# Kernel optimization log

Measured on AMD Instinct MI355X. Metric: run time of the kernel, lower is better.

The kernel has to match this reference:

```python
import jax, jax.numpy as jnp
import numpy as np

EPS = 1e-5
K = 9
DILATION = 1

def bn(x, g, b, m, v):
    # x: (B,C,N,1), inference-mode BatchNorm2d with running stats
    sh = (1, -1, 1, 1)
    return (x - m.reshape(sh)) * (g.reshape(sh) / jnp.sqrt(v.reshape(sh) + EPS)) + b.reshape(sh)

def conv1x1(x, w, b):
    # w: (Cout, Cin), x: (B,Cin,N,1)
    return jnp.einsum('oc,bcnj->bonj', w, x) + b.reshape(1, -1, 1, 1)

def knn_idx(feat, k):
    # feat: (B,C,N) -> (B,N,k) indices of k nearest nodes (incl. self)
    xt = jnp.transpose(feat, (0, 2, 1))  # (B,N,C)
    x2 = jnp.sum(xt * xt, axis=-1)       # (B,N)
    dist = x2[:, :, None] - 2.0 * jnp.einsum('bnc,bmc->bnm', xt, xt) + x2[:, None, :]
    _, idx = jax.lax.top_k(-dist, k)
    return idx

def setup_inputs():
    key = jax.random.key(0)
    ks = jax.random.split(key, 24)
    B, C, H, W = 16, 256, 32, 32
    HID = 512
    def g(i, shape, s=1.0):
        return jax.random.normal(ks[i], shape, dtype=jnp.float32) * s
    def pos(i, shape):
        return jax.random.uniform(ks[i], shape, dtype=jnp.float32, minval=0.5, maxval=1.5)
    return {
        'x': g(0, (B, C, H, W)),
        'fc1_w': g(1, (C, C), 0.05), 'fc1_b': g(2, (C,), 0.05),
        'bn1_g': pos(3, (C,)), 'bn1_b': g(4, (C,), 0.1), 'bn1_m': g(5, (C,), 0.1), 'bn1_v': pos(6, (C,)),
        'gc_w': g(7, (HID, 2 * C), 0.05), 'gc_b': g(8, (HID,), 0.05),
        'gbn_g': pos(9, (HID,)), 'gbn_b': g(10, (HID,), 0.1), 'gbn_m': g(11, (HID,), 0.1), 'gbn_v': pos(12, (HID,)),
        'bn2_g': pos(13, (HID,)), 'bn2_b': g(14, (HID,), 0.1), 'bn2_m': g(15, (HID,), 0.1), 'bn2_v': pos(16, (HID,)),
        'fc2_w': g(17, (C, HID), 0.05), 'fc2_b': g(18, (C,), 0.05),
        'bn3_g': pos(19, (C,)), 'bn3_b': g(20, (C,), 0.1), 'bn3_m': g(21, (C,), 0.1), 'bn3_v': pos(22, (C,)),
    }

def reference(x, fc1_w, fc1_b, bn1_g, bn1_b, bn1_m, bn1_v,
              gc_w, gc_b, gbn_g, gbn_b, gbn_m, gbn_v,
              bn2_g, bn2_b, bn2_m, bn2_v,
              fc2_w, fc2_b, bn3_g, bn3_b, bn3_m, bn3_v):
    B, C, H, W = x.shape
    N = H * W
    x = x.reshape(B, C, N, 1)
    shortcut = x
    # fc1: 1x1 conv + BN
    h = bn(conv1x1(x, fc1_w, fc1_b), bn1_g, bn1_b, bn1_m, bn1_v)
    # DyGraphConv2d: dynamic dilated kNN graph over N nodes
    feat = h[..., 0]  # (B,C,N)
    idx = knn_idx(feat, K * DILATION)[:, :, ::DILATION]  # (B,N,K)
    # MRConv2d: max over neighbors of (x_j - x_i)
    x_j = jax.vmap(lambda f, i: f[:, i])(feat, idx)        # (B,C,N,K) gather
    diff_max = jnp.max(x_j - feat[:, :, :, None], axis=-1)  # (B,C,N)
    # interleave [x, max_diff] along channel dim -> (B, 2C, N, 1)
    m = jnp.stack([feat, diff_max], axis=2).reshape(B, 2 * C, N, 1)
    g = conv1x1(m, gc_w, gc_b)
    g = bn(g, gbn_g, gbn_b, gbn_m, gbn_v)  # BasicConv BN, act='None'
    # graph_conv Sequential: BN + GELU (erf, torch default)
    g = jax.nn.gelu(bn(g, bn2_g, bn2_b, bn2_m, bn2_v), approximate=False)
    # fc2 + residual (drop_path=0 -> identity)
    out = bn(conv1x1(g, fc2_w, fc2_b), bn3_g, bn3_b, bn3_m, bn3_v)
    return out + shortcut
```

## Files before the change

kernel.cpp:

```cpp
#include <hip/hip_runtime.h>
#include <hip/hip_bf16.h>
#include <stdint.h>

typedef unsigned long long u64;
typedef __hip_bfloat16 bf16;
typedef short s8v __attribute__((ext_vector_type(8)));
typedef short s4v __attribute__((ext_vector_type(4)));
typedef float f4v __attribute__((ext_vector_type(4)));

#define B_   16
#define C_   256
#define N_   1024
#define HID_ 512

__device__ __forceinline__ unsigned short f2b(float f) {
    unsigned u = __float_as_uint(f);
    unsigned r = (u + 0x7FFFu + ((u >> 16) & 1u)) >> 16;
    return (unsigned short)r;
}
__device__ __forceinline__ float b2f(unsigned short s) {
    return __uint_as_float(((unsigned)s) << 16);
}
__device__ __forceinline__ float ldIn(const void* p, long long i, int bf) {
    return bf ? b2f(((const unsigned short*)p)[i]) : ((const float*)p)[i];
}
__device__ __forceinline__ u64 shfl_xor_u64(u64 v, int m) {
    unsigned lo = (unsigned)v, hi = (unsigned)(v >> 32);
    lo = __shfl_xor(lo, m, 64);
    hi = __shfl_xor(hi, m, 64);
    return ((u64)hi << 32) | lo;
}
__device__ __forceinline__ int probe_bf16(const void* xp) {
    const unsigned short* u = (const unsigned short*)xp;
    int cnt = 0;
    for (int i = 0; i < 64; ++i) {
        int e = (u[2 * i] >> 7) & 0xFF;
        cnt += (e >= 87 && e <= 167);
    }
    return (cnt >= 48) ? 1 : 0;
}

__global__ __launch_bounds__(256)
void prep_cast(const void* xp,
    const void* wg, const void* w2,
    const void* fc1_b, const void* bn1_g, const void* bn1_b, const void* bn1_m, const void* bn1_v,
    const void* gc_b,  const void* gbn_g, const void* gbn_b, const void* gbn_m, const void* gbn_v,
    const void* bn2_g, const void* bn2_b, const void* bn2_m, const void* bn2_v,
    const void* fc2_b, const void* bn3_g, const void* bn3_b, const void* bn3_m, const void* bn3_v,
    int* flags, float* s1, float* t1, float* Sg, float* Tg, float* s3, float* t3,
    short* Wgb, short* W2b)
{
    __shared__ int sf;
    int t = threadIdx.x, blk = blockIdx.x;
    if (t == 0) sf = probe_bf16(xp);
    __syncthreads();
    int bf = sf;

    if (blk == 0) {
        if (t == 0) flags[0] = bf;
        for (int i = t; i < 512; i += 256) {
            if (i < 256) {
                float g = ldIn(bn1_g, i, bf), bb = ldIn(bn1_b, i, bf);
                float m = ldIn(bn1_m, i, bf), v  = ldIn(bn1_v, i, bf);
                float s = g / sqrtf(v + 1e-5f);
                s1[i] = s;
                t1[i] = (ldIn(fc1_b, i, bf) - m) * s + bb;

                float g3 = ldIn(bn3_g, i, bf), b3 = ldIn(bn3_b, i, bf);
                float m3 = ldIn(bn3_m, i, bf), v3 = ldIn(bn3_v, i, bf);
                float ss3 = g3 / sqrtf(v3 + 1e-5f);
                s3[i] = ss3;
                t3[i] = (ldIn(fc2_b, i, bf) - m3) * ss3 + b3;
            }
            float gg = ldIn(gbn_g, i, bf), gb = ldIn(gbn_b, i, bf);
            float gm = ldIn(gbn_m, i, bf), gv = ldIn(gbn_v, i, bf);
            float sg = gg / sqrtf(gv + 1e-5f);
            float g2 = ldIn(bn2_g, i, bf), b2 = ldIn(bn2_b, i, bf);
            float m2 = ldIn(bn2_m, i, bf), v2 = ldIn(bn2_v, i, bf);
            float s2 = g2 / sqrtf(v2 + 1e-5f);
            Sg[i] = sg * s2;
            Tg[i] = ((ldIn(gc_b, i, bf) - gm) * sg + gb - m2) * s2 + b2;
        }
    }

    #pragma unroll
    for (int e = 0; e < 2; ++e) {
        int i = (blk * 256 + t) * 2 + e;
        if (i < 262144) {
            Wgb[i] = (short)f2b(ldIn(wg, i, bf));
        } else if (i < 393216) {
            int j = i - 262144;
            W2b[j] = (short)f2b(ldIn(w2, j, bf));
        }
    }
}

__global__ __launch_bounds__(256)
void fc1_valu(const void* __restrict__ Aw, const void* __restrict__ Bx,
              float* __restrict__ Ft, const float* __restrict__ s1,
              const float* __restrict__ t1, const int* __restrict__ flags)
{
    __shared__ float As[16][68];
    __shared__ float Bs[16][68];

    int inf = flags[0];
    int b  = blockIdx.z;
    int o0 = blockIdx.y * 64, n0 = blockIdx.x * 64;
    int t  = threadIdx.x;
    int tn = t & 15, to = t >> 4;
    long long bbase = (long long)b * C_ * N_;

    float acc[4][4] = {};

    for (int k0 = 0; k0 < C_; k0 += 16) {
        {
            int l = t * 4;
            int ao = l >> 4, ak = l & 15;
            long long ai = (long long)(o0 + ao) * C_ + k0 + ak;
            As[ak + 0][ao] = ldIn(Aw, ai + 0, inf);
            As[ak + 1][ao] = ldIn(Aw, ai + 1, inf);
            As[ak + 2][ao] = ldIn(Aw, ai + 2, inf);
            As[ak + 3][ao] = ldIn(Aw, ai + 3, inf);
        }
        {
            int l = t * 4;
            int bk = l >> 6, bn = l & 63;
            long long bi = bbase + (long long)(k0 + bk) * N_ + n0 + bn;
            Bs[bk][bn + 0] = ldIn(Bx, bi + 0, inf);
            Bs[bk][bn + 1] = ldIn(Bx, bi + 1, inf);
            Bs[bk][bn + 2] = ldIn(Bx, bi + 2, inf);
            Bs[bk][bn + 3] = ldIn(Bx, bi + 3, inf);
        }
        __syncthreads();
        #pragma unroll
        for (int k = 0; k < 16; ++k) {
            float av[4], bv[4];
            #pragma unroll
            for (int i = 0; i < 4; ++i) av[i] = As[k][to * 4 + i];
            #pragma unroll
            for (int j = 0; j < 4; ++j) bv[j] = Bs[k][tn * 4 + j];
            #pragma unroll
            for (int i = 0; i < 4; ++i)
                #pragma unroll
                for (int j = 0; j < 4; ++j) acc[i][j] += av[i] * bv[j];
        }
        __syncthreads();
    }

    #pragma unroll
    for (int i = 0; i < 4; ++i) {
        int o = o0 + to * 4 + i;
        float s = s1[o], tt = t1[o];
        #pragma unroll
        for (int j = 0; j < 4; ++j) {
            int n = n0 + tn * 4 + j;
            Ft[((long long)(b << 10) + n) * C_ + o] = acc[i][j] * s + tt;
        }
    }
}

__global__ __launch_bounds__(256)
void prep_F(const float* __restrict__ Ft, short* __restrict__ Fhi,
            short* __restrict__ Flo, float* __restrict__ x2)
{
    int t = threadIdx.x;
    int wv = t >> 6, lane = t & 63;
    int n = blockIdx.x * 4 + wv;
    int b = blockIdx.y;
    long long base = ((long long)(b << 10) + n) * C_ + lane * 4;
    f4v f = *(const f4v*)(Ft + base);

    s4v hi, lo;
    #pragma unroll
    for (int r = 0; r < 4; ++r) {
        unsigned short h = f2b(f[r]);
        hi[r] = (short)h;
        lo[r] = (short)f2b(f[r] - b2f(h));
    }
    *(s4v*)(Fhi + base) = hi;
    *(s4v*)(Flo + base) = lo;

    float ss = f[0]*f[0] + f[1]*f[1] + f[2]*f[2] + f[3]*f[3];
    #pragma unroll
    for (int s = 32; s >= 1; s >>= 1) ss += __shfl_xor(ss, s, 64);
    if (lane == 0) x2[(b << 10) + n] = ss;
}

__global__ __launch_bounds__(256)
void gram_topk(const short* __restrict__ Fhi, const short* __restrict__ Flo,
               const float* __restrict__ x2, u64* __restrict__ Part)
{
    __shared__ __align__(16) char ldsbuf[31232];
    short* Ah  = (short*)(ldsbuf);
    short* Al  = (short*)(ldsbuf + 10240);
    short* Bh  = (short*)(ldsbuf + 20480);
    short* Bl  = (short*)(ldsbuf + 25600);
    float* x2s = (float*)(ldsbuf + 30720);
    u64*   mrg  = (u64*)(ldsbuf);
    u64*   mrg2 = (u64*)(ldsbuf + 20480);

    int t = threadIdx.x;
    int q0 = blockIdx.x * 64, mq = blockIdx.y, b = blockIdx.z;
    int wv = t >> 6, ln15 = t & 15, quad = (t >> 4) & 3;

    if (t < 128) x2s[t] = x2[(b << 10) + mq * 128 + t];

    f4v acc[8];
    #pragma unroll
    for (int i = 0; i < 8; ++i) acc[i] = 0.f;

    for (int kc = 0; kc < 8; ++kc) {
        __syncthreads();
        #pragma unroll
        for (int s = 0; s < 6; ++s) {
            int sid = t + s * 256;
            int row = sid >> 2, seg = sid & 3;
            const short* src;
            short* dst;
            int grow;
            if (row < 128)      { dst = &Ah[row * 40 + seg * 8];         grow = mq * 128 + row;       src = Fhi; }
            else if (row < 256) { dst = &Al[(row - 128) * 40 + seg * 8]; grow = mq * 128 + row - 128; src = Flo; }
            else if (row < 320) { dst = &Bh[(row - 256) * 40 + seg * 8]; grow = q0 + row - 256;       src = Fhi; }
            else                { dst = &Bl[(row - 320) * 40 + seg * 8]; grow = q0 + row - 320;       src = Flo; }
            *(s8v*)dst = *(const s8v*)(src + ((long long)((b << 10) + grow)) * C_ + kc * 32 + seg * 8);
        }
        __syncthreads();
        s8v qh = *(s8v*)&Bh[(wv * 16 + ln15) * 40 + quad * 8];
        s8v ql = *(s8v*)&Bl[(wv * 16 + ln15) * 40 + quad * 8];
        #pragma unroll
        for (int i = 0; i < 8; ++i) {
            s8v mh = *(s8v*)&Ah[(i * 16 + ln15) * 40 + quad * 8];
            s8v ml = *(s8v*)&Al[(i * 16 + ln15) * 40 + quad * 8];
            acc[i] = __builtin_amdgcn_mfma_f32_16x16x32_bf16(mh, qh, acc[i], 0, 0, 0);
            acc[i] = __builtin_amdgcn_mfma_f32_16x16x32_bf16(mh, ql, acc[i], 0, 0, 0);
            acc[i] = __builtin_amdgcn_mfma_f32_16x16x32_bf16(ml, qh, acc[i], 0, 0, 0);
        }
    }

    u64 l[9];
    #pragma unroll
    for (int i = 0; i < 9; ++i) l[i] = ~0ULL;
    #pragma unroll
    for (int i = 0; i < 8; ++i) {
        #pragma unroll
        for (int r = 0; r < 4; ++r) {
            int mloc = i * 16 + quad * 4 + r;
            float d = x2s[mloc] - 2.f * acc[i][r];
            unsigned u = __float_as_uint(d);
            u = (u & 0x80000000u) ? ~u : (u | 0x80000000u);
            u64 key = ((u64)u << 32) | (unsigned)(mq * 128 + mloc);
            if (key < l[8]) {
                u64 x = key;
                #pragma unroll
                for (int jj = 0; jj < 9; ++jj) {
                    u64 lo2 = l[jj] < x ? l[jj] : x;
                    u64 hi2 = l[jj] < x ? x : l[jj];
                    l[jj] = lo2; x = hi2;
                }
            }
        }
    }

    __syncthreads();
    {
        int qloc = wv * 16 + ln15;
        #pragma unroll
        for (int k = 0; k < 9; ++k) mrg[(qloc * 4 + quad) * 9 + k] = l[k];
    }
    __syncthreads();
    if (t < 128) {
        int r = t >> 1, pr = t & 1;
        const u64* LA = &mrg[(r * 4 + pr * 2) * 9];
        const u64* LB = LA + 9;
        int ia = 0, ib = 0;
        u64* Po = &mrg2[(r * 2 + pr) * 9];
        #pragma unroll
        for (int k = 0; k < 9; ++k) {
            u64 va = LA[ia], vb = LB[ib];
            bool ta = va < vb;
            Po[k] = ta ? va : vb;
            ia += ta; ib += !ta;
        }
    }
    __syncthreads();
    if (t < 64) {
        const u64* LA = &mrg2[(t * 2) * 9];
        const u64* LB = LA + 9;
        int ia = 0, ib = 0;
        u64* P = Part + (((long long)((b << 10) + q0 + t)) * 8 + mq) * 9;
        #pragma unroll
        for (int k = 0; k < 9; ++k) {
            u64 va = LA[ia], vb = LB[ib];
            bool ta = va < vb;
            P[k] = ta ? va : vb;
            ia += ta; ib += !ta;
        }
    }
}

__global__ __launch_bounds__(256)
void build_Mt(const float* __restrict__ Ft, const u64* __restrict__ Part,
              short* __restrict__ Mt)
{
    int t = threadIdx.x;
    int wv = t >> 6, lane = t & 63;
    int n = blockIdx.x * 4 + wv;
    int b = blockIdx.y;
    long long nb = (long long)(b << 10) + n;

    const u64* L = Part + nb * 72 + (long long)(lane & 7) * 9;
    u64 l[9];
    #pragma unroll
    for (int k = 0; k < 9; ++k) l[k] = L[k];
    #pragma unroll
    for (int s = 1; s <= 4; s <<= 1) {
        u64 p[9];
        #pragma unroll
        for (int k = 0; k < 9; ++k) p[k] = shfl_xor_u64(l[k], s);
        #pragma unroll
        for (int k = 0; k < 9; ++k) {
            u64 x = p[k];
            if (x < l[8]) {
                #pragma unroll
                for (int jj = 0; jj < 9; ++jj) {
                    u64 lo2 = l[jj] < x ? l[jj] : x;
                    u64 hi2 = l[jj] < x ? x : l[jj];
                    l[jj] = lo2; x = hi2;
                }
            }
        }
    }

    int c0 = lane * 4;
    f4v f = *(const f4v*)(Ft + nb * C_ + c0);
    f4v mx = {-3.4e38f, -3.4e38f, -3.4e38f, -3.4e38f};
    #pragma unroll
    for (int k = 0; k < 9; ++k) {
        int id = (int)(l[k] & 0xFFFFFFFFu);
        f4v g = *(const f4v*)(Ft + ((long long)(b << 10) + id) * C_ + c0);
        mx[0] = fmaxf(mx[0], g[0]); mx[1] = fmaxf(mx[1], g[1]);
        mx[2] = fmaxf(mx[2], g[2]); mx[3] = fmaxf(mx[3], g[3]);
    }
    s8v m8;
    #pragma unroll
    for (int r = 0; r < 4; ++r) {
        m8[2 * r]     = (short)f2b(f[r]);
        m8[2 * r + 1] = (short)f2b(mx[r] - f[r]);
    }
    *(s8v*)(Mt + nb * (2 * C_) + 2 * c0) = m8;
}

template<int EPI>
__global__ __launch_bounds__(256)
void mfma_gemm(const short* __restrict__ A, const short* __restrict__ Bm,
               void* __restrict__ Out, const float* __restrict__ scale,
               const float* __restrict__ bias, const void* __restrict__ resid,
               const int* __restrict__ flags, int K, int Odim)
{
    __shared__ __align__(16) short As[64 * 40];
    __shared__ __align__(16) short Bs[64 * 40];

    int t = threadIdx.x, b = blockIdx.z;
    int n0 = blockIdx.x * 64, o0 = blockIdx.y * 64;
    int wv = t >> 6, ln15 = t & 15, quad = (t >> 4) & 3;

    f4v acc[4];
    #pragma unroll
    for (int i = 0; i < 4; ++i) acc[i] = 0.f;

    int nkc = K >> 5;
    for (int kc = 0; kc < nkc; ++kc) {
        __syncthreads();
        #pragma unroll
        for (int s = 0; s < 2; ++s) {
            int sid = t + s * 256;
            int row = (sid >> 2) & 63, seg = sid & 3;
            if (s == 0)
                *(s8v*)&As[row * 40 + seg * 8] =
                    *(const s8v*)(A + (long long)(o0 + row) * K + kc * 32 + seg * 8);
            else
                *(s8v*)&Bs[row * 40 + seg * 8] =
                    *(const s8v*)(Bm + ((long long)((b << 10) + n0 + row)) * K + kc * 32 + seg * 8);
        }
        __syncthreads();
        s8v bf = *(s8v*)&Bs[(wv * 16 + ln15) * 40 + quad * 8];
        #pragma unroll
        for (int i = 0; i < 4; ++i) {
            s8v a = *(s8v*)&As[(i * 16 + ln15) * 40 + quad * 8];
            acc[i] = __builtin_amdgcn_mfma_f32_16x16x32_bf16(a, bf, acc[i], 0, 0, 0);
        }
    }

    int inf = flags[0];
    int n = n0 + wv * 16 + ln15;
    #pragma unroll
    for (int i = 0; i < 4; ++i) {
        int ob = o0 + i * 16 + quad * 4;
        if (EPI == 0) {
            s4v g;
            #pragma unroll
            for (int r = 0; r < 4; ++r) {
                float val = acc[i][r] * scale[ob + r] + bias[ob + r];
                val = 0.5f * val * (1.0f + erff(val * 0.70710678118654752f));
                g[r] = (short)f2b(val);
            }
            *(s4v*)((short*)Out + ((long long)((b << 10) + n)) * Odim + ob) = g;
        } else {
            #pragma unroll
            for (int r = 0; r < 4; ++r) {
                int o = ob + r;
                long long oi = ((long long)b * Odim + o) * N_ + n;
                ((float*)Out)[oi] = acc[i][r] * scale[o] + bias[o] + ldIn(resid, oi, inf);
            }
        }
    }
}

extern "C" void kernel_launch(void* const* d_in, const int* in_sizes, int n_in,
                              void* d_out, int out_size, void* d_ws, size_t ws_size,
                              hipStream_t stream)
{
    const void* p[23];
    if (n_in >= 23 && in_sizes[0] != 4194304 && in_sizes[22] == 4194304) {
        const int amap[23] = {
            22, 13, 12, 1, 0, 2, 3,
            21, 20, 17, 16, 18, 19,
            5, 4, 6, 7,
            15, 14, 9, 8, 10, 11 };
        for (int i = 0; i < 23; ++i) p[i] = d_in[amap[i]];
    } else {
        for (int i = 0; i < 23; ++i) p[i] = d_in[i];
    }

    const void* x     = p[0];
    const void* fc1_w = p[1];
    const void* fc1_b = p[2];
    const void* bn1_g = p[3];
    const void* bn1_b = p[4];
    const void* bn1_m = p[5];
    const void* bn1_v = p[6];
    const void* gc_w  = p[7];
    const void* gc_b  = p[8];
    const void* gbn_g = p[9];
    const void* gbn_b = p[10];
    const void* gbn_m = p[11];
    const void* gbn_v = p[12];
    const void* bn2_g = p[13];
    const void* bn2_b = p[14];
    const void* bn2_m = p[15];
    const void* bn2_v = p[16];
    const void* fc2_w = p[17];
    const void* fc2_b = p[18];
    const void* bn3_g = p[19];
    const void* bn3_b = p[20];
    const void* bn3_m = p[21];
    const void* bn3_v = p[22];

    char* ws = (char*)d_ws;
    size_t off = 0;
    int*   flags = (int*)ws;
    float* s1 = (float*)(ws + 256);
    float* t1 = s1 + 256;
    float* s3 = t1 + 256;
    float* t3 = s3 + 256;
    float* Sg = t3 + 256;
    float* Tg = Sg + 512;
    off = 16384;
    short* Wgb   = (short*)(ws + off); off += (size_t)HID_ * 2 * C_ * 2;
    short* W2b   = (short*)(ws + off); off += (size_t)C_ * HID_ * 2;
    float* Ft    = (float*)(ws + off); off += (size_t)B_ * N_ * C_ * 4;
    short* Fhi   = (short*)(ws + off); off += (size_t)B_ * N_ * C_ * 2;
    short* Flo   = (short*)(ws + off); off += (size_t)B_ * N_ * C_ * 2;
    float* x2    = (float*)(ws + off); off += (size_t)B_ * N_ * 4;
    u64*   Part  = (u64*)  (ws + off); off += (size_t)B_ * N_ * 8 * 9 * 8;
    short* Mt    = (short*)(ws + off); off += (size_t)B_ * N_ * 2 * C_ * 2;
    short* Gt    = (short*)(ws + off); off += (size_t)B_ * N_ * HID_ * 2;

    prep_cast<<<768, 256, 0, stream>>>(x,
        gc_w, fc2_w,
        fc1_b, bn1_g, bn1_b, bn1_m, bn1_v,
        gc_b, gbn_g, gbn_b, gbn_m, gbn_v,
        bn2_g, bn2_b, bn2_m, bn2_v,
        fc2_b, bn3_g, bn3_b, bn3_m, bn3_v,
        flags, s1, t1, Sg, Tg, s3, t3,
        Wgb, W2b);

    fc1_valu<<<dim3(16, 4, B_), 256, 0, stream>>>(fc1_w, x, Ft, s1, t1, flags);

    prep_F<<<dim3(N_ / 4, B_), 256, 0, stream>>>(Ft, Fhi, Flo, x2);

    gram_topk<<<dim3(16, 8, 16), 256, 0, stream>>>(Fhi, Flo, x2, Part);

    build_Mt<<<dim3(256, 16), 256, 0, stream>>>(Ft, Part, Mt);

    mfma_gemm<0><<<dim3(16, 8, 16), 256, 0, stream>>>(
        Wgb, Mt, Gt, Sg, Tg, nullptr, flags, 2 * C_, HID_);

    mfma_gemm<1><<<dim3(16, 4, 16), 256, 0, stream>>>(
        W2b, Gt, d_out, s3, t3, x, flags, HID_, C_);
}
```

Before: 320.4 us.

## Load per-wave B operands directly from global and merge top-k via shuffles

```diff
diff --git a/kernel.cpp b/kernel.cpp
--- a/kernel.cpp
+++ b/kernel.cpp
@@ -190,14 +190,10 @@
 void gram_topk(const short* __restrict__ Fhi, const short* __restrict__ Flo,
                const float* __restrict__ x2, u64* __restrict__ Part)
 {
-    __shared__ __align__(16) char ldsbuf[31232];
+    __shared__ __align__(16) char ldsbuf[20992];
     short* Ah  = (short*)(ldsbuf);
     short* Al  = (short*)(ldsbuf + 10240);
-    short* Bh  = (short*)(ldsbuf + 20480);
-    short* Bl  = (short*)(ldsbuf + 25600);
-    float* x2s = (float*)(ldsbuf + 30720);
-    u64*   mrg  = (u64*)(ldsbuf);
-    u64*   mrg2 = (u64*)(ldsbuf + 20480);
+    float* x2s = (float*)(ldsbuf + 20480);
 
     int t = threadIdx.x;
     int q0 = blockIdx.x * 64, mq = blockIdx.y, b = blockIdx.z;
@@ -205,28 +201,28 @@
 
     if (t < 128) x2s[t] = x2[(b << 10) + mq * 128 + t];
 
+    long long qbase = ((long long)((b << 10) + q0 + wv * 16 + ln15)) * C_ + quad * 8;
+
     f4v acc[8];
     #pragma unroll
     for (int i = 0; i < 8; ++i) acc[i] = 0.f;
 
     for (int kc = 0; kc < 8; ++kc) {
-        __syncthreads();
-        #pragma unroll
-        for (int s = 0; s < 6; ++s) {
+        s8v qh = *(const s8v*)(Fhi + qbase + kc * 32);
+        s8v ql = *(const s8v*)(Flo + qbase + kc * 32);
+        __syncthreads();
+        #pragma unroll
+        for (int s = 0; s < 4; ++s) {
             int sid = t + s * 256;
             int row = sid >> 2, seg = sid & 3;
-            const short* src;
-            short* dst;
-            int grow;
-            if (row < 128)      { dst = &Ah[row * 40 + seg * 8];         grow = mq * 128 + row;       src = Fhi; }
-            else if (row < 256) { dst = &Al[(row - 128) * 40 + seg * 8]; grow = mq * 128 + row - 128; src = Flo; }
-            else if (row < 320) { dst = &Bh[(row - 256) * 40 + seg * 8]; grow = q0 + row - 256;       src = Fhi; }
-            else                { dst = &Bl[(row - 320) * 40 + seg * 8]; grow = q0 + row - 320;       src = Flo; }
-            *(s8v*)dst = *(const s8v*)(src + ((long long)((b << 10) + grow)) * C_ + kc * 32 + seg * 8);
-        }
-        __syncthreads();
-        s8v qh = *(s8v*)&Bh[(wv * 16 + ln15) * 40 + quad * 8];
-        s8v ql = *(s8v*)&Bl[(wv * 16 + ln15) * 40 + quad * 8];
+            if (row < 128)
+                *(s8v*)&Ah[row * 40 + seg * 8] =
+                    *(const s8v*)(Fhi + ((long long)((b << 10) + mq * 128 + row)) * C_ + kc * 32 + seg * 8);
+            else
+                *(s8v*)&Al[(row - 128) * 40 + seg * 8] =
+                    *(const s8v*)(Flo + ((long long)((b << 10) + mq * 128 + row - 128)) * C_ + kc * 32 + seg * 8);
+        }
+        __syncthreads();
         #pragma unroll
         for (int i = 0; i < 8; ++i) {
             s8v mh = *(s8v*)&Ah[(i * 16 + ln15) * 40 + quad * 8];
@@ -261,59 +257,8 @@
         }
     }
 
-    __syncthreads();
-    {
-        int qloc = wv * 16 + ln15;
-        #pragma unroll
-        for (int k = 0; k < 9; ++k) mrg[(qloc * 4 + quad) * 9 + k] = l[k];
-    }
-    __syncthreads();
-    if (t < 128) {
-        int r = t >> 1, pr = t & 1;
-        const u64* LA = &mrg[(r * 4 + pr * 2) * 9];
-        const u64* LB = LA + 9;
-        int ia = 0, ib = 0;
-        u64* Po = &mrg2[(r * 2 + pr) * 9];
-        #pragma unroll
-        for (int k = 0; k < 9; ++k) {
-            u64 va = LA[ia], vb = LB[ib];
-            bool ta = va < vb;
-            Po[k] = ta ? va : vb;
-            ia += ta; ib += !ta;
-        }
-    }
-    __syncthreads();
-    if (t < 64) {
-        const u64* LA = &mrg2[(t * 2) * 9];
-        const u64* LB = LA + 9;
-        int ia = 0, ib = 0;
-        u64* P = Part + (((long long)((b << 10) + q0 + t)) * 8 + mq) * 9;
-        #pragma unroll
-        for (int k = 0; k < 9; ++k) {
-            u64 va = LA[ia], vb = LB[ib];
-            bool ta = va < vb;
-            P[k] = ta ? va : vb;
-            ia += ta; ib += !ta;
-        }
-    }
-}
-
-__global__ __launch_bounds__(256)
-void build_Mt(const float* __restrict__ Ft, const u64* __restrict__ Part,
-              short* __restrict__ Mt)
-{
-    int t = threadIdx.x;
-    int wv = t >> 6, lane = t & 63;
-    int n = blockIdx.x * 4 + wv;
-    int b = blockIdx.y;
-    long long nb = (long long)(b << 10) + n;
-
-    const u64* L = Part + nb * 72 + (long long)(lane & 7) * 9;
-    u64 l[9];
-    #pragma unroll
-    for (int k = 0; k < 9; ++k) l[k] = L[k];
-    #pragma unroll
-    for (int s = 1; s <= 4; s <<= 1) {
+    #pragma unroll
+    for (int s = 16; s <= 32; s <<= 1) {
         u64 p[9];
         #pragma unroll
         for (int k = 0; k < 9; ++k) p[k] = shfl_xor_u64(l[k], s);
@@ -331,6 +276,46 @@
         }
     }
 
+    if (quad == 0) {
+        u64* P = Part + (((long long)((b << 10) + q0 + wv * 16 + ln15)) * 8 + mq) * 9;
+        #pragma unroll
+        for (int k = 0; k < 9; ++k) P[k] = l[k];
+    }
+}
+
+__global__ __launch_bounds__(256)
+void build_Mt(const float* __restrict__ Ft, const u64* __restrict__ Part,
+              short* __restrict__ Mt)
+{
+    int t = threadIdx.x;
+    int wv = t >> 6, lane = t & 63;
+    int n = blockIdx.x * 4 + wv;
+    int b = blockIdx.y;
+    long long nb = (long long)(b << 10) + n;
+
+    const u64* L = Part + nb * 72 + (long long)(lane & 7) * 9;
+    u64 l[9];
+    #pragma unroll
+    for (int k = 0; k < 9; ++k) l[k] = L[k];
+    #pragma unroll
+    for (int s = 1; s <= 4; s <<= 1) {
+        u64 p[9];
+        #pragma unroll
+        for (int k = 0; k < 9; ++k) p[k] = shfl_xor_u64(l[k], s);
+        #pragma unroll
+        for (int k = 0; k < 9; ++k) {
+            u64 x = p[k];
+            if (x < l[8]) {
+                #pragma unroll
+                for (int jj = 0; jj < 9; ++jj) {
+                    u64 lo2 = l[jj] < x ? l[jj] : x;
+                    u64 hi2 = l[jj] < x ? x : l[jj];
+                    l[jj] = lo2; x = hi2;
+                }
+            }
+        }
+    }
+
     int c0 = lane * 4;
     f4v f = *(const f4v*)(Ft + nb * C_ + c0);
     f4v mx = {-3.4e38f, -3.4e38f, -3.4e38f, -3.4e38f};
@@ -358,32 +343,27 @@
                const int* __restrict__ flags, int K, int Odim)
 {
     __shared__ __align__(16) short As[64 * 40];
-    __shared__ __align__(16) short Bs[64 * 40];
 
     int t = threadIdx.x, b = blockIdx.z;
     int n0 = blockIdx.x * 64, o0 = blockIdx.y * 64;
     int wv = t >> 6, ln15 = t & 15, quad = (t >> 4) & 3;
 
+    long long nbase = ((long long)((b << 10) + n0 + wv * 16 + ln15)) * K + quad * 8;
+
     f4v acc[4];
     #pragma unroll
     for (int i = 0; i < 4; ++i) acc[i] = 0.f;
 
     int nkc = K >> 5;
     for (int kc = 0; kc < nkc; ++kc) {
-        __syncthreads();
-        #pragma unroll
-        for (int s = 0; s < 2; ++s) {
-            int sid = t + s * 256;
-            int row = (sid >> 2) & 63, seg = sid & 3;
-            if (s == 0)
-                *(s8v*)&As[row * 40 + seg * 8] =
-                    *(const s8v*)(A + (long long)(o0 + row) * K + kc * 32 + seg * 8);
-            else
-                *(s8v*)&Bs[row * 40 + seg * 8] =
-                    *(const s8v*)(Bm + ((long long)((b << 10) + n0 + row)) * K + kc * 32 + seg * 8);
-        }
-        __syncthreads();
-        s8v bf = *(s8v*)&Bs[(wv * 16 + ln15) * 40 + quad * 8];
+        s8v bf = *(const s8v*)(Bm + nbase + kc * 32);
+        __syncthreads();
+        {
+            int row = t >> 2, seg = t & 3;
+            *(s8v*)&As[row * 40 + seg * 8] =
+                *(const s8v*)(A + (long long)(o0 + row) * K + kc * 32 + seg * 8);
+        }
+        __syncthreads();
         #pragma unroll
         for (int i = 0; i < 4; ++i) {
             s8v a = *(s8v*)&As[(i * 16 + ln15) * 40 + quad * 8];
```

Measured after the change: 329.8 us. +2.9%, slower.
